# Kernel tuning notes

Measured on AMD Instinct MI355X. Metric: run time of the kernel, lower is better.

The kernel has to match this reference:

```python
import jax, jax.numpy as jnp
from jax import lax
import numpy as np

D = 128      # embedding_dim == GRU input_size == hidden_size
B, S, L = 256, 32, 32  # users, slates per user, slate length


def setup_inputs() -> dict:
    key = jax.random.key(0)
    ks = jax.random.split(key, 8)
    sc = 1.0 / np.sqrt(D)  # PyTorch GRU/Linear init scale
    return {
        "item_embs": jax.random.normal(ks[0], (B, S, L, D), jnp.float32),
        "user_embs": jax.random.normal(ks[1], (B, S, D), jnp.float32),
        "W_ih": jax.random.normal(ks[2], (3 * D, D), jnp.float32) * sc,
        "W_hh": jax.random.normal(ks[3], (3 * D, D), jnp.float32) * sc,
        "b_ih": jax.random.normal(ks[4], (3 * D,), jnp.float32) * sc,
        "b_hh": jax.random.normal(ks[5], (3 * D,), jnp.float32) * sc,
        "W_out": jax.random.normal(ks[6], (1, D), jnp.float32) * sc,
        "b_out": jax.random.normal(ks[7], (1,), jnp.float32) * sc,
    }


def reference(item_embs, user_embs, W_ih, W_hh, b_ih, b_hh, W_out, b_out):
    b, s, l, d = item_embs.shape
    x = item_embs.reshape(b * s, l, d)          # [N, L, D]
    h0 = user_embs.reshape(b * s, d)            # [N, D] initial hidden per slate

    # Precompute input-side gate projections for all timesteps (one big GEMM).
    gx = jnp.einsum('nld,gd->nlg', x, W_ih) + b_ih  # [N, L, 3D], PyTorch gate order r,z,n

    def step(h, gx_t):
        gh = h @ W_hh.T + b_hh                   # [N, 3D]
        xr, xz, xn = jnp.split(gx_t, 3, axis=-1)
        hr, hz, hn = jnp.split(gh, 3, axis=-1)
        r = jax.nn.sigmoid(xr + hr)
        z = jax.nn.sigmoid(xz + hz)
        n = jnp.tanh(xn + r * hn)
        h_new = (1.0 - z) * n + z * h
        return h_new, h_new

    _, hs = lax.scan(step, h0, jnp.swapaxes(gx, 0, 1))  # hs: [L, N, D]
    rnn_out = jnp.swapaxes(hs, 0, 1)             # [N, L, D]
    out = rnn_out @ W_out.T + b_out              # [N, L, 1]
    return out.reshape(b, s, l)
```

## Files before the change

### kernel.cpp

```cpp
#include <hip/hip_runtime.h>
#include <math.h>

#define DD   128
#define LL   32
#define MS   32
#define NT   512
#define NSEQ 8192
#define XHP  264
#define OLP  36

typedef short bf16x8 __attribute__((ext_vector_type(8)));
typedef float f32x4  __attribute__((ext_vector_type(4)));

__device__ __forceinline__ unsigned short f2bf(float f) {
    unsigned u = __float_as_uint(f);
    u += 0x7fffu + ((u >> 16) & 1u);
    return (unsigned short)(u >> 16);
}

#if __has_builtin(__builtin_amdgcn_cvt_pk_bf16_f32)
typedef __bf16 bf16x2_t __attribute__((ext_vector_type(2)));
__device__ __forceinline__ unsigned pack2(float a, float b) {
    union { bf16x2_t v; unsigned u; } c;
    c.v = __builtin_amdgcn_cvt_pk_bf16_f32(a, b);
    return c.u;
}
#else
__device__ __forceinline__ unsigned pack2(float a, float b) {
    return (unsigned)f2bf(a) | ((unsigned)f2bf(b) << 16);
}
#endif

__device__ __forceinline__ void pack8(float4 a, float4 b, unsigned short* dst) {
    union { unsigned u[4]; bf16x8 v; } pk;
    pk.u[0] = pack2(a.x, a.y); pk.u[1] = pack2(a.z, a.w);
    pk.u[2] = pack2(b.x, b.y); pk.u[3] = pack2(b.z, b.w);
    *(bf16x8*)dst = pk.v;
}

__device__ __forceinline__ float fast_rcp(float x) {
    return __builtin_amdgcn_rcpf(x);
}

__global__ void prep_weights(const float* __restrict__ Wih,
                             const float* __restrict__ Whh,
                             unsigned short* __restrict__ Wfrag) {
    int idx = blockIdx.x * blockDim.x + threadIdx.x;
    int j    = idx & 7;
    int lane = (idx >> 3) & 63;
    int kk   = (idx >> 9) & 7;
    int ct   = idx >> 12;
    int n = lane & 15, q = lane >> 4;
    float v = 0.f;
    if (ct < 16) {
        int g = ct * 16 + n;
        int k = kk * 32 + q * 8 + j;
        v = (k < 128) ? Wih[g * 128 + k] : Whh[g * 128 + (k - 128)];
    } else if (ct < 24) {
        if (kk < 4) {
            int g = 256 + (ct - 16) * 16 + n;
            int k = kk * 32 + q * 8 + j;
            v = Wih[g * 128 + k];
        }
    } else {
        if (kk >= 4) {
            int g = 256 + (ct - 24) * 16 + n;
            int k = kk * 32 + q * 8 + j - 128;
            v = Whh[g * 128 + k];
        }
    }
    Wfrag[idx] = f2bf(v);
}

__global__ __launch_bounds__(NT, 2) void gru_mfma(
    const float* __restrict__ x,
    const float* __restrict__ h0,
    const unsigned short* __restrict__ Wfrag,
    const float* __restrict__ b_ih,
    const float* __restrict__ b_hh,
    const float* __restrict__ w_out,
    const float* __restrict__ b_out,
    float* __restrict__ out)
{
    __shared__ __align__(16) unsigned short xh[2][MS][XHP];
    __shared__ __align__(16) unsigned short wofl[4 * 64 * 8];
    __shared__ __align__(16) float outl[MS][OLP];

    const int tid  = threadIdx.x;
    const int n0   = blockIdx.x * MS;
    const int wv   = tid >> 6;
    const int lane = tid & 63;
    const int ln   = lane & 15;
    const int q    = lane >> 4;
    const int gn   = tid >> 4;
    const int gd8  = (tid & 15) * 8;
    const int d    = wv * 16 + ln;

    const float br  = b_ih[d]        + b_hh[d];
    const float bz  = b_ih[DD + d]   + b_hh[DD + d];
    const float bin = b_ih[2*DD + d];
    const float bhn = b_hh[2*DD + d];
    const float bo  = b_out[0];

    bf16x8 wrz0[8], wrz1[8], wxn[4], whn[4];
    {
        const bf16x8* W = (const bf16x8*)Wfrag;
        #pragma unroll
        for (int kk = 0; kk < 8; ++kk) {
            wrz0[kk] = W[((wv    ) * 8 + kk) * 64 + lane];
            wrz1[kk] = W[((wv + 8) * 8 + kk) * 64 + lane];
        }
        #pragma unroll
        for (int kk = 0; kk < 4; ++kk) {
            wxn[kk] = W[((wv + 16) * 8 + kk    ) * 64 + lane];
            whn[kk] = W[((wv + 24) * 8 + kk + 4) * 64 + lane];
        }
    }

    #pragma unroll
    for (int e = 0; e < 4; ++e) {
        int idx = tid * 4 + e;
        int j   = idx & 7;
        int l2  = (idx >> 3) & 63;
        int kk  = idx >> 9;
        int n2 = l2 & 15, q2 = l2 >> 4;
        wofl[idx] = (n2 == 0) ? f2bf(w_out[kk * 32 + q2 * 8 + j])
                              : (unsigned short)0;
    }

    float hprev[8];
    #pragma unroll
    for (int tl = 0; tl < 2; ++tl)
        #pragma unroll
        for (int i = 0; i < 4; ++i)
            hprev[tl*4+i] = h0[(size_t)(n0 + tl*16 + q*4 + i) * DD + d];

    {
        const float* hb = h0 + (size_t)(n0 + gn) * DD + gd8;
        pack8(*(const float4*)hb, *(const float4*)(hb + 4), &xh[0][gn][DD + gd8]);
    }
    const float* xbase = x + ((size_t)(n0 + gn) * LL) * DD + gd8;
    pack8(*(const float4*)xbase, *(const float4*)(xbase + 4), &xh[0][gn][gd8]);
    float4 xa0 = *(const float4*)(xbase + 1 * DD);
    float4 xa1 = *(const float4*)(xbase + 1 * DD + 4);
    float4 xb0 = *(const float4*)(xbase + 2 * DD);
    float4 xb1 = *(const float4*)(xbase + 2 * DD + 4);
    __syncthreads();

#define GRU_STEP(PAR, XR0, XR1, TCUR, TREFILL)                                 \
    {                                                                          \
                       \
        pack8(XR0, XR1, &xh[(PAR) ^ 1][gn][gd8]);                              \
        XR0 = *(const float4*)(xbase + (size_t)(TREFILL) * DD);                \
        XR1 = *(const float4*)(xbase + (size_t)(TREFILL) * DD + 4);            \
                 \
        f32x4 c0[2], c1[2], c2[2], c3[2];                                      \
        _Pragma("unroll")                                                      \
        for (int tl = 0; tl < 2; ++tl) {                                       \
            c0[tl] = (f32x4){0.f,0.f,0.f,0.f}; c1[tl] = c0[tl];                \
            c2[tl] = c0[tl]; c3[tl] = c0[tl];                                  \
        }                                                                      \
        const unsigned short* xr0 = &xh[PAR][ln][0];                           \
        const unsigned short* xr1 = &xh[PAR][16 + ln][0];                      \
        _Pragma("unroll")                                                      \
        for (int kk = 0; kk < 8; ++kk) {                                       \
            bf16x8 a0 = *(const bf16x8*)(xr0 + kk*32 + q*8);                   \
            bf16x8 a1 = *(const bf16x8*)(xr1 + kk*32 + q*8);                   \
            c0[0] = __builtin_amdgcn_mfma_f32_16x16x32_bf16(a0, wrz0[kk], c0[0],0,0,0); \
            c0[1] = __builtin_amdgcn_mfma_f32_16x16x32_bf16(a1, wrz0[kk], c0[1],0,0,0); \
            c1[0] = __builtin_amdgcn_mfma_f32_16x16x32_bf16(a0, wrz1[kk], c1[0],0,0,0); \
            c1[1] = __builtin_amdgcn_mfma_f32_16x16x32_bf16(a1, wrz1[kk], c1[1],0,0,0); \
            if (kk < 4) {                                                      \
                c2[0] = __builtin_amdgcn_mfma_f32_16x16x32_bf16(a0, wxn[kk], c2[0],0,0,0); \
                c2[1] = __builtin_amdgcn_mfma_f32_16x16x32_bf16(a1, wxn[kk], c2[1],0,0,0); \
            } else {                                                           \
                c3[0] = __builtin_amdgcn_mfma_f32_16x16x32_bf16(a0, whn[kk-4], c3[0],0,0,0); \
                c3[1] = __builtin_amdgcn_mfma_f32_16x16x32_bf16(a1, whn[kk-4], c3[1],0,0,0); \
            }                                                                  \
        }                                                                      \
             \
        if (wv < 2 && (TCUR) > 0) {                                            \
            f32x4 c4 = {0.f,0.f,0.f,0.f};                                      \
            const unsigned short* xr = (wv == 0) ? xr0 : xr1;                  \
            _Pragma("unroll")                                                  \
            for (int kk = 0; kk < 4; ++kk) {                                   \
                bf16x8 a = *(const bf16x8*)(xr + (kk+4)*32 + q*8);             \
                bf16x8 b = *(const bf16x8*)&wofl[(kk*64 + lane)*8];            \
                c4 = __builtin_amdgcn_mfma_f32_16x16x32_bf16(a, b, c4,0,0,0);  \
            }                                                                  \
            if (ln == 0) {                                                     \
                _Pragma("unroll")                                              \
                for (int i = 0; i < 4; ++i)                                    \
                    outl[wv*16 + q*4 + i][(TCUR)-1] = c4[i] + bo;              \
            }                                                                  \
        }                                                                      \
                       \
        _Pragma("unroll")                                                      \
        for (int tl = 0; tl < 2; ++tl) {                                       \
            _Pragma("unroll")                                                  \
            for (int i = 0; i < 4; ++i) {                                      \
                const float rr = fast_rcp(1.f + __expf(-(c0[tl][i] + br)));    \
                const float zz = fast_rcp(1.f + __expf(-(c1[tl][i] + bz)));    \
                float aa = c2[tl][i] + bin + rr * (c3[tl][i] + bhn);           \
                aa = fminf(fmaxf(aa, -20.f), 20.f);                            \
                const float ee = __expf(-2.f * aa);                            \
                const float th = (1.f - ee) * fast_rcp(1.f + ee);              \
                const float hh = th + zz * (hprev[tl*4+i] - th);               \
                hprev[tl*4+i] = hh;                                            \
                xh[(PAR) ^ 1][tl*16 + q*4 + i][DD + d] = f2bf(hh);             \
            }                                                                  \
        }                                                                      \
        __syncthreads();                                                       \
    }

    for (int t = 0; t < LL; t += 2) {
        const int r0 = (t + 3 < LL) ? t + 3 : LL - 1;
        const int r1 = (t + 4 < LL) ? t + 4 : LL - 1;
        GRU_STEP(0, xa0, xa1, t,     r0)
        GRU_STEP(1, xb0, xb1, t + 1, r1)
    }
#undef GRU_STEP

    if (wv < 2) {
        f32x4 c4 = {0.f,0.f,0.f,0.f};
        const unsigned short* xr = &xh[0][wv*16 + ln][0];
        #pragma unroll
        for (int kk = 0; kk < 4; ++kk) {
            bf16x8 a = *(const bf16x8*)(xr + (kk+4)*32 + q*8);
            bf16x8 b = *(const bf16x8*)&wofl[(kk*64 + lane)*8];
            c4 = __builtin_amdgcn_mfma_f32_16x16x32_bf16(a, b, c4,0,0,0);
        }
        if (ln == 0) {
            #pragma unroll
            for (int i = 0; i < 4; ++i)
                outl[wv*16 + q*4 + i][LL-1] = c4[i] + bo;
        }
    }
    __syncthreads();

    if (tid < 256) {
        const int row = tid >> 3;
        const int t4  = (tid & 7) * 4;
        float4 v = *(const float4*)&outl[row][t4];
        *(float4*)(out + (size_t)(n0 + row) * LL + t4) = v;
    }
}

extern "C" void kernel_launch(void* const* d_in, const int* in_sizes, int n_in,
                              void* d_out, int out_size, void* d_ws, size_t ws_size,
                              hipStream_t stream) {
    const float* item  = (const float*)d_in[0];
    const float* user  = (const float*)d_in[1];
    const float* W_ih  = (const float*)d_in[2];
    const float* W_hh  = (const float*)d_in[3];
    const float* b_ih  = (const float*)d_in[4];
    const float* b_hh  = (const float*)d_in[5];
    const float* W_out = (const float*)d_in[6];
    const float* b_out = (const float*)d_in[7];
    float* out = (float*)d_out;

    unsigned short* Wfrag = (unsigned short*)d_ws;

    prep_weights<<<512, 256, 0, stream>>>(W_ih, W_hh, Wfrag);
    gru_mfma<<<NSEQ / MS, NT, 0, stream>>>(item, user, Wfrag,
                                           b_ih, b_hh, W_out, b_out, out);
}
```

Measured before the change: 221.6 us.

## Warp-specialize GRU: producer waves compute input gates ahead of recurrent waves

The block grows to 1024 threads and is split into two roles. Eight waves run only the hidden-state recurrence, doing 24 MFMAs per step with the W_hh fragments kept in registers. The other eight waves load and convert x, compute the W_ih gate projections one step ahead into a double-buffered fp32 LDS buffer, and compute the output projection. This takes the input-side GEMM off the serial recurrence path, at the cost of about 155KB of dynamic LDS (one block per CU) and a producer/consumer handoff through barriers. The tanh clamp is dropped and the sigmoid/tanh form is slightly reworked.

Result: no change. 222.2 us (+0.2%).

```diff
diff --git a/kernel.cpp b/kernel.cpp
--- a/kernel.cpp
+++ b/kernel.cpp
@@ -4,13 +4,23 @@
 #define DD   128
 #define LL   32
 #define MS   32
-#define NT   512
+#define NT   1024
 #define NSEQ 8192
-#define XHP  264
+#define XP   136
+#define GP   36
 #define OLP  36
+
+#define GX_ELEMS   (384 * GP)
+#define SMEM_XH_X  (2 * 384 * GP * 4)
+#define SMEM_XH_H  (SMEM_XH_X + 2 * MS * XP * 2)
+#define SMEM_OUTL  (SMEM_XH_H + 2 * MS * XP * 2)
+#define SMEM_WOFL  (SMEM_OUTL + MS * OLP * 4)
+#define SMEM_TOTAL (SMEM_WOFL + 4 * 64 * 8 * 2)
 
 typedef short bf16x8 __attribute__((ext_vector_type(8)));
 typedef float f32x4  __attribute__((ext_vector_type(4)));
+
+#define MFMA __builtin_amdgcn_mfma_f32_16x16x32_bf16
 
 __device__ __forceinline__ unsigned short f2bf(float f) {
     unsigned u = __float_as_uint(f);
@@ -45,34 +55,21 @@
 __global__ void prep_weights(const float* __restrict__ Wih,
                              const float* __restrict__ Whh,
                              unsigned short* __restrict__ Wfrag) {
-    int idx = blockIdx.x * blockDim.x + threadIdx.x;
+    int idx  = blockIdx.x * blockDim.x + threadIdx.x;
     int j    = idx & 7;
     int lane = (idx >> 3) & 63;
-    int kk   = (idx >> 9) & 7;
-    int ct   = idx >> 12;
+    int kk   = (idx >> 9) & 3;
+    int sl   = (idx >> 11) & 7;
+    int sg   = idx >> 14;
     int n = lane & 15, q = lane >> 4;
-    float v = 0.f;
-    if (ct < 16) {
-        int g = ct * 16 + n;
-        int k = kk * 32 + q * 8 + j;
-        v = (k < 128) ? Wih[g * 128 + k] : Whh[g * 128 + (k - 128)];
-    } else if (ct < 24) {
-        if (kk < 4) {
-            int g = 256 + (ct - 16) * 16 + n;
-            int k = kk * 32 + q * 8 + j;
-            v = Wih[g * 128 + k];
-        }
-    } else {
-        if (kk >= 4) {
-            int g = 256 + (ct - 24) * 16 + n;
-            int k = kk * 32 + q * 8 + j - 128;
-            v = Whh[g * 128 + k];
-        }
-    }
-    Wfrag[idx] = f2bf(v);
-}
-
-__global__ __launch_bounds__(NT, 2) void gru_mfma(
+    int k  = kk * 32 + q * 8 + j;
+    int g  = (sg >= 3) ? sg - 3 : sg;
+    int gd = g * 128 + sl * 16 + n;
+    const float* src = (sg >= 3) ? Whh : Wih;
+    Wfrag[idx] = f2bf(src[gd * 128 + k]);
+}
+
+__global__ __launch_bounds__(NT, 4) void gru_mfma(
     const float* __restrict__ x,
     const float* __restrict__ h0,
     const unsigned short* __restrict__ Wfrag,
@@ -82,9 +79,12 @@
     const float* __restrict__ b_out,
     float* __restrict__ out)
 {
-    __shared__ __align__(16) unsigned short xh[2][MS][XHP];
-    __shared__ __align__(16) unsigned short wofl[4 * 64 * 8];
-    __shared__ __align__(16) float outl[MS][OLP];
+    extern __shared__ char smem[];
+    float*          gxs  = (float*)(smem);
+    unsigned short* xhx  = (unsigned short*)(smem + SMEM_XH_X);
+    unsigned short* xhh  = (unsigned short*)(smem + SMEM_XH_H);
+    float*          outl = (float*)(smem + SMEM_OUTL);
+    unsigned short* wofl = (unsigned short*)(smem + SMEM_WOFL);
 
     const int tid  = threadIdx.x;
     const int n0   = blockIdx.x * MS;
@@ -92,157 +92,233 @@
     const int lane = tid & 63;
     const int ln   = lane & 15;
     const int q    = lane >> 4;
-    const int gn   = tid >> 4;
-    const int gd8  = (tid & 15) * 8;
-    const int d    = wv * 16 + ln;
-
-    const float br  = b_ih[d]        + b_hh[d];
-    const float bz  = b_ih[DD + d]   + b_hh[DD + d];
-    const float bin = b_ih[2*DD + d];
-    const float bhn = b_hh[2*DD + d];
-    const float bo  = b_out[0];
-
-    bf16x8 wrz0[8], wrz1[8], wxn[4], whn[4];
-    {
-        const bf16x8* W = (const bf16x8*)Wfrag;
-        #pragma unroll
-        for (int kk = 0; kk < 8; ++kk) {
-            wrz0[kk] = W[((wv    ) * 8 + kk) * 64 + lane];
-            wrz1[kk] = W[((wv + 8) * 8 + kk) * 64 + lane];
-        }
+    const bf16x8* W = (const bf16x8*)Wfrag;
+
+    if (wv < 8) {
+        const int d = wv * 16 + ln;
+        const float bhr = b_hh[d], bhz = b_hh[DD + d], bhn = b_hh[2*DD + d];
+
+        bf16x8 whr[4], whz[4], whn[4];
         #pragma unroll
         for (int kk = 0; kk < 4; ++kk) {
-            wxn[kk] = W[((wv + 16) * 8 + kk    ) * 64 + lane];
-            whn[kk] = W[((wv + 24) * 8 + kk + 4) * 64 + lane];
-        }
-    }
-
-    #pragma unroll
-    for (int e = 0; e < 4; ++e) {
-        int idx = tid * 4 + e;
-        int j   = idx & 7;
-        int l2  = (idx >> 3) & 63;
-        int kk  = idx >> 9;
-        int n2 = l2 & 15, q2 = l2 >> 4;
-        wofl[idx] = (n2 == 0) ? f2bf(w_out[kk * 32 + q2 * 8 + j])
-                              : (unsigned short)0;
-    }
-
-    float hprev[8];
-    #pragma unroll
-    for (int tl = 0; tl < 2; ++tl)
+            whr[kk] = W[((24 + wv)*4 + kk)*64 + lane];
+            whz[kk] = W[((32 + wv)*4 + kk)*64 + lane];
+            whn[kk] = W[((40 + wv)*4 + kk)*64 + lane];
+        }
+
         #pragma unroll
-        for (int i = 0; i < 4; ++i)
-            hprev[tl*4+i] = h0[(size_t)(n0 + tl*16 + q*4 + i) * DD + d];
-
-    {
-        const float* hb = h0 + (size_t)(n0 + gn) * DD + gd8;
-        pack8(*(const float4*)hb, *(const float4*)(hb + 4), &xh[0][gn][DD + gd8]);
-    }
-    const float* xbase = x + ((size_t)(n0 + gn) * LL) * DD + gd8;
-    pack8(*(const float4*)xbase, *(const float4*)(xbase + 4), &xh[0][gn][gd8]);
-    float4 xa0 = *(const float4*)(xbase + 1 * DD);
-    float4 xa1 = *(const float4*)(xbase + 1 * DD + 4);
-    float4 xb0 = *(const float4*)(xbase + 2 * DD);
-    float4 xb1 = *(const float4*)(xbase + 2 * DD + 4);
-    __syncthreads();
-
-#define GRU_STEP(PAR, XR0, XR1, TCUR, TREFILL)                                 \
-    {                                                                          \
-                       \
-        pack8(XR0, XR1, &xh[(PAR) ^ 1][gn][gd8]);                              \
-        XR0 = *(const float4*)(xbase + (size_t)(TREFILL) * DD);                \
-        XR1 = *(const float4*)(xbase + (size_t)(TREFILL) * DD + 4);            \
-                 \
-        f32x4 c0[2], c1[2], c2[2], c3[2];                                      \
-        _Pragma("unroll")                                                      \
-        for (int tl = 0; tl < 2; ++tl) {                                       \
-            c0[tl] = (f32x4){0.f,0.f,0.f,0.f}; c1[tl] = c0[tl];                \
-            c2[tl] = c0[tl]; c3[tl] = c0[tl];                                  \
-        }                                                                      \
-        const unsigned short* xr0 = &xh[PAR][ln][0];                           \
-        const unsigned short* xr1 = &xh[PAR][16 + ln][0];                      \
-        _Pragma("unroll")                                                      \
-        for (int kk = 0; kk < 8; ++kk) {                                       \
-            bf16x8 a0 = *(const bf16x8*)(xr0 + kk*32 + q*8);                   \
-            bf16x8 a1 = *(const bf16x8*)(xr1 + kk*32 + q*8);                   \
-            c0[0] = __builtin_amdgcn_mfma_f32_16x16x32_bf16(a0, wrz0[kk], c0[0],0,0,0); \
-            c0[1] = __builtin_amdgcn_mfma_f32_16x16x32_bf16(a1, wrz0[kk], c0[1],0,0,0); \
-            c1[0] = __builtin_amdgcn_mfma_f32_16x16x32_bf16(a0, wrz1[kk], c1[0],0,0,0); \
-            c1[1] = __builtin_amdgcn_mfma_f32_16x16x32_bf16(a1, wrz1[kk], c1[1],0,0,0); \
-            if (kk < 4) {                                                      \
-                c2[0] = __builtin_amdgcn_mfma_f32_16x16x32_bf16(a0, wxn[kk], c2[0],0,0,0); \
-                c2[1] = __builtin_amdgcn_mfma_f32_16x16x32_bf16(a1, wxn[kk], c2[1],0,0,0); \
-            } else {                                                           \
-                c3[0] = __builtin_amdgcn_mfma_f32_16x16x32_bf16(a0, whn[kk-4], c3[0],0,0,0); \
-                c3[1] = __builtin_amdgcn_mfma_f32_16x16x32_bf16(a1, whn[kk-4], c3[1],0,0,0); \
-            }                                                                  \
-        }                                                                      \
-             \
-        if (wv < 2 && (TCUR) > 0) {                                            \
-            f32x4 c4 = {0.f,0.f,0.f,0.f};                                      \
-            const unsigned short* xr = (wv == 0) ? xr0 : xr1;                  \
-            _Pragma("unroll")                                                  \
-            for (int kk = 0; kk < 4; ++kk) {                                   \
-                bf16x8 a = *(const bf16x8*)(xr + (kk+4)*32 + q*8);             \
-                bf16x8 b = *(const bf16x8*)&wofl[(kk*64 + lane)*8];            \
-                c4 = __builtin_amdgcn_mfma_f32_16x16x32_bf16(a, b, c4,0,0,0);  \
-            }                                                                  \
-            if (ln == 0) {                                                     \
-                _Pragma("unroll")                                              \
-                for (int i = 0; i < 4; ++i)                                    \
-                    outl[wv*16 + q*4 + i][(TCUR)-1] = c4[i] + bo;              \
-            }                                                                  \
-        }                                                                      \
-                       \
-        _Pragma("unroll")                                                      \
-        for (int tl = 0; tl < 2; ++tl) {                                       \
-            _Pragma("unroll")                                                  \
-            for (int i = 0; i < 4; ++i) {                                      \
-                const float rr = fast_rcp(1.f + __expf(-(c0[tl][i] + br)));    \
-                const float zz = fast_rcp(1.f + __expf(-(c1[tl][i] + bz)));    \
-                float aa = c2[tl][i] + bin + rr * (c3[tl][i] + bhn);           \
-                aa = fminf(fmaxf(aa, -20.f), 20.f);                            \
-                const float ee = __expf(-2.f * aa);                            \
-                const float th = (1.f - ee) * fast_rcp(1.f + ee);              \
-                const float hh = th + zz * (hprev[tl*4+i] - th);               \
-                hprev[tl*4+i] = hh;                                            \
-                xh[(PAR) ^ 1][tl*16 + q*4 + i][DD + d] = f2bf(hh);             \
-            }                                                                  \
-        }                                                                      \
-        __syncthreads();                                                       \
-    }
-
-    for (int t = 0; t < LL; t += 2) {
-        const int r0 = (t + 3 < LL) ? t + 3 : LL - 1;
-        const int r1 = (t + 4 < LL) ? t + 4 : LL - 1;
-        GRU_STEP(0, xa0, xa1, t,     r0)
-        GRU_STEP(1, xb0, xb1, t + 1, r1)
-    }
-#undef GRU_STEP
-
-    if (wv < 2) {
-        f32x4 c4 = {0.f,0.f,0.f,0.f};
-        const unsigned short* xr = &xh[0][wv*16 + ln][0];
+        for (int e = 0; e < 4; ++e) {
+            int idx = tid * 4 + e;
+            int j   = idx & 7;
+            int l2  = (idx >> 3) & 63;
+            int kk  = idx >> 9;
+            int n2 = l2 & 15, q2 = l2 >> 4;
+            wofl[idx] = (n2 == 0) ? f2bf(w_out[kk * 32 + q2 * 8 + j])
+                                  : (unsigned short)0;
+        }
+        {
+            const int gn = tid >> 4, gd8 = (tid & 15) * 8;
+            const float* hb = h0 + (size_t)(n0 + gn) * DD + gd8;
+            pack8(*(const float4*)hb, *(const float4*)(hb + 4),
+                  &xhh[gn * XP + gd8]);
+        }
+        float hprev[8];
+        #pragma unroll
+        for (int tl = 0; tl < 2; ++tl)
+            #pragma unroll
+            for (int i = 0; i < 4; ++i)
+                hprev[tl*4+i] = h0[(size_t)(n0 + tl*16 + q*4 + i) * DD + d];
+
+        __syncthreads();
+        __syncthreads();
+
+        for (int t = 0; t < LL; ++t) {
+            const int sl_ = t & 1;
+            const float* gr = gxs + sl_ * GX_ELEMS;
+            f32x4 cr[2], cz[2], ch[2];
+            #pragma unroll
+            for (int tl = 0; tl < 2; ++tl) {
+                const int co = tl*16 + q*4;
+                cr[tl] = *(const f32x4*)&gr[(d)*GP + co];
+                cz[tl] = *(const f32x4*)&gr[(DD + d)*GP + co];
+                ch[tl] = (f32x4){0.f, 0.f, 0.f, 0.f};
+            }
+            const unsigned short* hr0 = &xhh[sl_*MS*XP + ln*XP];
+            const unsigned short* hr1 = hr0 + 16*XP;
+            #pragma unroll
+            for (int kk = 0; kk < 4; ++kk) {
+                bf16x8 a0 = *(const bf16x8*)(hr0 + kk*32 + q*8);
+                bf16x8 a1 = *(const bf16x8*)(hr1 + kk*32 + q*8);
+                cr[0] = MFMA(a0, whr[kk], cr[0], 0,0,0);
+                cr[1] = MFMA(a1, whr[kk], cr[1], 0,0,0);
+                cz[0] = MFMA(a0, whz[kk], cz[0], 0,0,0);
+                cz[1] = MFMA(a1, whz[kk], cz[1], 0,0,0);
+                ch[0] = MFMA(a0, whn[kk], ch[0], 0,0,0);
+                ch[1] = MFMA(a1, whn[kk], ch[1], 0,0,0);
+            }
+            f32x4 gnx[2];
+            #pragma unroll
+            for (int tl = 0; tl < 2; ++tl)
+                gnx[tl] = *(const f32x4*)&gr[(2*DD + d)*GP + tl*16 + q*4];
+
+            unsigned short* hw = xhh + (sl_ ^ 1)*MS*XP;
+            #pragma unroll
+            for (int tl = 0; tl < 2; ++tl)
+                #pragma unroll
+                for (int i = 0; i < 4; ++i) {
+                    const float rr = fast_rcp(1.f + __expf(-(cr[tl][i] + bhr)));
+                    const float zz = fast_rcp(1.f + __expf(-(cz[tl][i] + bhz)));
+                    const float aa = gnx[tl][i] + rr * (ch[tl][i] + bhn);
+                    const float ee = __expf(-2.f * aa);
+                    const float th = 2.f * fast_rcp(1.f + ee) - 1.f;
+                    const float hh = th + zz * (hprev[tl*4+i] - th);
+                    hprev[tl*4+i] = hh;
+                    hw[(tl*16 + q*4 + i)*XP + d] = f2bf(hh);
+                }
+            __syncthreads();
+        }
+        __syncthreads();
+
+        if (tid < 256) {
+            const int row = tid >> 3;
+            const int t4  = (tid & 7) * 4;
+            float4 v = *(const float4*)&outl[row * OLP + t4];
+            *(float4*)(out + (size_t)(n0 + row) * LL + t4) = v;
+        }
+    } else {
+        const int pv = wv - 8;
+        const int dp = pv * 16 + ln;
+        const float bir  = b_ih[dp];
+        const float biz  = b_ih[DD + dp];
+        const float bin_ = b_ih[2*DD + dp];
+        const float bo   = b_out[0];
+
+        bf16x8 wxr[4], wxz[4], wxn[4];
         #pragma unroll
         for (int kk = 0; kk < 4; ++kk) {
-            bf16x8 a = *(const bf16x8*)(xr + (kk+4)*32 + q*8);
-            bf16x8 b = *(const bf16x8*)&wofl[(kk*64 + lane)*8];
-            c4 = __builtin_amdgcn_mfma_f32_16x16x32_bf16(a, b, c4,0,0,0);
-        }
-        if (ln == 0) {
-            #pragma unroll
-            for (int i = 0; i < 4; ++i)
-                outl[wv*16 + q*4 + i][LL-1] = c4[i] + bo;
-        }
-    }
-    __syncthreads();
-
-    if (tid < 256) {
-        const int row = tid >> 3;
-        const int t4  = (tid & 7) * 4;
-        float4 v = *(const float4*)&outl[row][t4];
-        *(float4*)(out + (size_t)(n0 + row) * LL + t4) = v;
+            wxr[kk] = W[((0  + pv)*4 + kk)*64 + lane];
+            wxz[kk] = W[((8  + pv)*4 + kk)*64 + lane];
+            wxn[kk] = W[((16 + pv)*4 + kk)*64 + lane];
+        }
+
+        const int pt  = tid & 511;
+        const int gn  = pt >> 4;
+        const int gd8 = (pt & 15) * 8;
+        const float* xbase = x + ((size_t)(n0 + gn) * LL) * DD + gd8;
+
+        pack8(*(const float4*)(xbase), *(const float4*)(xbase + 4),
+              &xhx[gn * XP + gd8]);
+        pack8(*(const float4*)(xbase + DD), *(const float4*)(xbase + DD + 4),
+              &xhx[MS*XP + gn * XP + gd8]);
+
+        __syncthreads();
+
+        {
+            const unsigned short* xr0 = &xhx[ln * XP];
+            const unsigned short* xr1 = xr0 + 16*XP;
+            f32x4 ar[2], az[2], an[2];
+            #pragma unroll
+            for (int tl = 0; tl < 2; ++tl) {
+                ar[tl] = (f32x4){bir, bir, bir, bir};
+                az[tl] = (f32x4){biz, biz, biz, biz};
+                an[tl] = (f32x4){bin_, bin_, bin_, bin_};
+            }
+            #pragma unroll
+            for (int kk = 0; kk < 4; ++kk) {
+                bf16x8 a0 = *(const bf16x8*)(xr0 + kk*32 + q*8);
+                bf16x8 a1 = *(const bf16x8*)(xr1 + kk*32 + q*8);
+                ar[0] = MFMA(a0, wxr[kk], ar[0], 0,0,0);
+                ar[1] = MFMA(a1, wxr[kk], ar[1], 0,0,0);
+                az[0] = MFMA(a0, wxz[kk], az[0], 0,0,0);
+                az[1] = MFMA(a1, wxz[kk], az[1], 0,0,0);
+                an[0] = MFMA(a0, wxn[kk], an[0], 0,0,0);
+                an[1] = MFMA(a1, wxn[kk], an[1], 0,0,0);
+            }
+            #pragma unroll
+            for (int tl = 0; tl < 2; ++tl) {
+                const int co = tl*16 + q*4;
+                *(f32x4*)&gxs[(dp)*GP + co]        = ar[tl];
+                *(f32x4*)&gxs[(DD + dp)*GP + co]   = az[tl];
+                *(f32x4*)&gxs[(2*DD + dp)*GP + co] = an[tl];
+            }
+        }
+        __syncthreads();
+
+        for (int t = 0; t < LL; ++t) {
+            float4 sa, sb;
+            const int ts = t + 2;
+            if (ts < LL) {
+                sa = *(const float4*)(xbase + (size_t)ts * DD);
+                sb = *(const float4*)(xbase + (size_t)ts * DD + 4);
+            }
+            if (t + 1 < LL) {
+                const int sr = (t + 1) & 1;
+                const unsigned short* xr0 = &xhx[sr*MS*XP + ln * XP];
+                const unsigned short* xr1 = xr0 + 16*XP;
+                f32x4 ar[2], az[2], an[2];
+                #pragma unroll
+                for (int tl = 0; tl < 2; ++tl) {
+                    ar[tl] = (f32x4){bir, bir, bir, bir};
+                    az[tl] = (f32x4){biz, biz, biz, biz};
+                    an[tl] = (f32x4){bin_, bin_, bin_, bin_};
+                }
+                #pragma unroll
+                for (int kk = 0; kk < 4; ++kk) {
+                    bf16x8 a0 = *(const bf16x8*)(xr0 + kk*32 + q*8);
+                    bf16x8 a1 = *(const bf16x8*)(xr1 + kk*32 + q*8);
+                    ar[0] = MFMA(a0, wxr[kk], ar[0], 0,0,0);
+                    ar[1] = MFMA(a1, wxr[kk], ar[1], 0,0,0);
+                    az[0] = MFMA(a0, wxz[kk], az[0], 0,0,0);
+                    az[1] = MFMA(a1, wxz[kk], az[1], 0,0,0);
+                    an[0] = MFMA(a0, wxn[kk], an[0], 0,0,0);
+                    an[1] = MFMA(a1, wxn[kk], an[1], 0,0,0);
+                }
+                float* gw = gxs + sr * GX_ELEMS;
+                #pragma unroll
+                for (int tl = 0; tl < 2; ++tl) {
+                    const int co = tl*16 + q*4;
+                    *(f32x4*)&gw[(dp)*GP + co]        = ar[tl];
+                    *(f32x4*)&gw[(DD + dp)*GP + co]   = az[tl];
+                    *(f32x4*)&gw[(2*DD + dp)*GP + co] = an[tl];
+                }
+            }
+            if (pv < 2 && t >= 1) {
+                f32x4 c4 = (f32x4){bo, bo, bo, bo};
+                const unsigned short* hrw = &xhh[(t & 1)*MS*XP + (pv*16 + ln)*XP];
+                #pragma unroll
+                for (int kk = 0; kk < 4; ++kk) {
+                    bf16x8 a = *(const bf16x8*)(hrw + kk*32 + q*8);
+                    bf16x8 b = *(const bf16x8*)&wofl[(kk*64 + lane)*8];
+                    c4 = MFMA(a, b, c4, 0,0,0);
+                }
+                if (ln == 0) {
+                    #pragma unroll
+                    for (int i = 0; i < 4; ++i)
+                        outl[(pv*16 + q*4 + i)*OLP + (t - 1)] = c4[i];
+                }
+            }
+            if (ts < LL)
+                pack8(sa, sb, &xhx[(t & 1)*MS*XP + gn * XP + gd8]);
+
+            __syncthreads();
+        }
+
+        if (pv < 2) {
+            f32x4 c4 = (f32x4){bo, bo, bo, bo};
+            const unsigned short* hrw = &xhh[(pv*16 + ln)*XP];
+            #pragma unroll
+            for (int kk = 0; kk < 4; ++kk) {
+                bf16x8 a = *(const bf16x8*)(hrw + kk*32 + q*8);
+                bf16x8 b = *(const bf16x8*)&wofl[(kk*64 + lane)*8];
+                c4 = MFMA(a, b, c4, 0,0,0);
+            }
+            if (ln == 0) {
+                #pragma unroll
+                for (int i = 0; i < 4; ++i)
+                    outl[(pv*16 + q*4 + i)*OLP + (LL - 1)] = c4[i];
+            }
+        }
+        __syncthreads();
     }
 }
 
@@ -261,7 +337,15 @@
 
     unsigned short* Wfrag = (unsigned short*)d_ws;
 
-    prep_weights<<<512, 256, 0, stream>>>(W_ih, W_hh, Wfrag);
-    gru_mfma<<<NSEQ / MS, NT, 0, stream>>>(item, user, Wfrag,
-                                           b_ih, b_hh, W_out, b_out, out);
-}
+    static bool smem_cfg = false;
+    if (!smem_cfg) {
+        hipFuncSetAttribute((const void*)gru_mfma,
+                            hipFuncAttributeMaxDynamicSharedMemorySize,
+                            SMEM_TOTAL);
+        smem_cfg = true;
+    }
+
+    prep_weights<<<384, 256, 0, stream>>>(W_ih, W_hh, Wfrag);
+    gru_mfma<<<NSEQ / MS, NT, SMEM_TOTAL, stream>>>(item, user, Wfrag,
+                                                    b_ih, b_hh, W_out, b_out, out);
+}
```
